# Kernel optimization log

Measured on AMD Instinct MI355X. Metric: run time of the kernel, lower is better.

## Reference

```python
import jax, jax.numpy as jnp
import numpy as np

Q_DIM = 64

def setup_inputs() -> dict:
    key = jax.random.key(0)
    k1, k2, k3, k4 = jax.random.split(key, 4)
    B, T, C, D = 2, 4096, 1024, Q_DIM
    x = jax.random.normal(k1, (B, T, C), dtype=jnp.float32)
    Wq = jax.random.normal(k2, (C, D), dtype=jnp.float32) * (C ** -0.5)
    Wk = jax.random.normal(k3, (C, D), dtype=jnp.float32) * (C ** -0.5)
    Wv = jax.random.normal(k4, (C, D), dtype=jnp.float32) * (C ** -0.5)
    return {"x": x, "Wq": Wq, "Wk": Wk, "Wv": Wv}

def reference(x, Wq, Wk, Wv):
    # x: [B,T,C]; Wq/Wk/Wv: [C,D]
    T = x.shape[1]
    D = Wq.shape[1]
    q = x @ Wq  # [B,T,D]
    k = x @ Wk
    v = x @ Wv
    scale = D ** -0.5
    aff = jnp.einsum('bqd,bkd->bqk', q, k) * scale  # [B,T,T]
    causal = jnp.tril(jnp.ones((T, T), dtype=bool))
    aff = jnp.where(causal, aff, -jnp.inf)
    attn = jax.nn.softmax(aff, axis=-1)
    out = jnp.einsum('bqk,bkd->bqd', attn, v)  # [B,T,D]
    return out
```

## Files before the change

### kernel.cpp

```cpp
#include <hip/hip_runtime.h>

typedef __bf16 bf16_t;
typedef __bf16 bf16x8 __attribute__((ext_vector_type(8)));
typedef __bf16 bf16x4 __attribute__((ext_vector_type(4)));
typedef float  f32x4  __attribute__((ext_vector_type(4)));
typedef _Float16 f16_t;
typedef _Float16 f16x8 __attribute__((ext_vector_type(8)));

#define TSEQ 4096
#define SEGS 8

__device__ __forceinline__ void barrier_lds() {
    __builtin_amdgcn_sched_barrier(0);
    asm volatile("s_waitcnt lgkmcnt(0)" ::: "memory");
    __builtin_amdgcn_s_barrier();
    __builtin_amdgcn_sched_barrier(0);
}

__global__ __launch_bounds__(256) void wsplit_k(
    const float* __restrict__ Wq, const float* __restrict__ Wk,
    const float* __restrict__ Wv, bf16_t* __restrict__ wT)
{
    __shared__ bf16_t th[64][72];
    const int mat = blockIdx.x >> 4;
    const int kb  = (blockIdx.x & 15) * 64;
    const float* W = (mat == 0) ? Wq : ((mat == 1) ? Wk : Wv);
    const float scale = (mat == 0) ? 0.18033688011112042f : 1.0f;
    const int t  = threadIdx.x;
    const int kl = t >> 2;
    const int dc = (t & 3) * 16;
    #pragma unroll
    for (int i = 0; i < 4; ++i) {
        float4 v = *reinterpret_cast<const float4*>(W + (long)(kb + kl) * 64 + dc + 4 * i);
        th[dc + 4*i + 0][kl] = (bf16_t)(v.x * scale);
        th[dc + 4*i + 1][kl] = (bf16_t)(v.y * scale);
        th[dc + 4*i + 2][kl] = (bf16_t)(v.z * scale);
        th[dc + 4*i + 3][kl] = (bf16_t)(v.w * scale);
    }
    __syncthreads();
    const int d  = t >> 2;
    const int kc = (t & 3) * 16;
    bf16x8 a0 = *reinterpret_cast<const bf16x8*>(&th[d][kc]);
    bf16x8 a1 = *reinterpret_cast<const bf16x8*>(&th[d][kc + 8]);
    long o = (long)(mat * 64 + d) * 1024 + kb + kc;
    *reinterpret_cast<bf16x8*>(wT + o)     = a0;
    *reinterpret_cast<bf16x8*>(wT + o + 8) = a1;
}

__global__ __launch_bounds__(256, 2) void proj_mfma(
    const float* __restrict__ X, const bf16_t* __restrict__ wT,
    bf16_t* __restrict__ qh, bf16_t* __restrict__ kh, bf16_t* __restrict__ vt)
{
    __shared__ __align__(16) unsigned char smem[27648];
    bf16_t (*wl)[96][72] = reinterpret_cast<bf16_t(*)[96][72]>(smem);
    float  (*vtl)[36]    = reinterpret_cast<float(*)[36]>(smem);

    const int tid = threadIdx.x, lane = tid & 63;
    const int w   = tid >> 6;
    const int mw  = w >> 1, nw2 = w & 1;
    const int q4 = lane & 15, g = lane >> 4;
    const int bx = blockIdx.x;
    const int rg = bx & 255, nb = bx >> 8;
    const long R0 = (long)rg * 32;

    const float* xrow = X + (R0 + 16 * mw + q4) * 1024 + 8 * g;

    const int wrow = tid >> 1, c32 = (tid & 1) * 32;
    const bf16_t* wsrc = wT + (long)(96 * nb + wrow) * 1024 + c32;
    const bool wact = (tid < 192);

    bf16x8 wr0, wr1, wr2, wr3;
    float4 xE[4], xO[4];
    f32x4 acc[3] = {};

    auto loadW = [&](int t) {
        if (wact) {
            wr0 = *reinterpret_cast<const bf16x8*>(wsrc + t * 64);
            wr1 = *reinterpret_cast<const bf16x8*>(wsrc + t * 64 + 8);
            wr2 = *reinterpret_cast<const bf16x8*>(wsrc + t * 64 + 16);
            wr3 = *reinterpret_cast<const bf16x8*>(wsrc + t * 64 + 24);
        }
    };
    auto writeW = [&](int buf) {
        if (wact) {
            *reinterpret_cast<bf16x8*>(&wl[buf][wrow][c32])      = wr0;
            *reinterpret_cast<bf16x8*>(&wl[buf][wrow][c32 + 8])  = wr1;
            *reinterpret_cast<bf16x8*>(&wl[buf][wrow][c32 + 16]) = wr2;
            *reinterpret_cast<bf16x8*>(&wl[buf][wrow][c32 + 24]) = wr3;
        }
    };
    auto loadX = [&](int t, float4 (&xc)[4]) {
        xc[0] = *reinterpret_cast<const float4*>(xrow + t * 64);
        xc[1] = *reinterpret_cast<const float4*>(xrow + t * 64 + 4);
        xc[2] = *reinterpret_cast<const float4*>(xrow + t * 64 + 32);
        xc[3] = *reinterpret_cast<const float4*>(xrow + t * 64 + 36);
    };

    loadW(0); writeW(0);
    loadW(1);
    loadX(0, xE); loadX(1, xO);
    asm volatile("" ::: "memory");
    barrier_lds();

    auto stepf = [&](int t, float4 (&xc)[4]) {
        if (t + 1 < 16) {
            writeW((t + 1) & 1);
            loadW(t + 2 < 16 ? t + 2 : 15);
        }
        bf16x8 a0 = {(bf16_t)xc[0].x, (bf16_t)xc[0].y, (bf16_t)xc[0].z, (bf16_t)xc[0].w,
                     (bf16_t)xc[1].x, (bf16_t)xc[1].y, (bf16_t)xc[1].z, (bf16_t)xc[1].w};
        bf16x8 a1 = {(bf16_t)xc[2].x, (bf16_t)xc[2].y, (bf16_t)xc[2].z, (bf16_t)xc[2].w,
                     (bf16_t)xc[3].x, (bf16_t)xc[3].y, (bf16_t)xc[3].z, (bf16_t)xc[3].w};
        if (t + 2 < 16) loadX(t + 2, xc);
        asm volatile("" ::: "memory");
        __builtin_amdgcn_s_setprio(1);
        #pragma unroll
        for (int j = 0; j < 3; ++j) {
            const int lr = (3 * nw2 + j) * 16 + q4;
            bf16x8 b0 = *reinterpret_cast<const bf16x8*>(&wl[t & 1][lr][8 * g]);
            bf16x8 b1 = *reinterpret_cast<const bf16x8*>(&wl[t & 1][lr][8 * g + 32]);
            acc[j] = __builtin_amdgcn_mfma_f32_16x16x32_bf16(a0, b0, acc[j], 0, 0, 0);
            acc[j] = __builtin_amdgcn_mfma_f32_16x16x32_bf16(a1, b1, acc[j], 0, 0, 0);
        }
        __builtin_amdgcn_s_setprio(0);
        barrier_lds();
    };
    #pragma unroll
    for (int tt = 0; tt < 16; tt += 2) { stepf(tt, xE); stepf(tt + 1, xO); }

    #pragma unroll
    for (int j = 0; j < 3; ++j) {
        const int nt = 6 * nb + 3 * nw2 + j;
        #pragma unroll
        for (int r = 0; r < 4; ++r) {
            const long row = R0 + 16 * mw + 4 * g + r;
            const float vv = acc[j][r];
            if (nt < 4)      qh[row * 64 + nt * 16 + q4] = (bf16_t)vv;
            else if (nt < 8) kh[row * 64 + (nt - 4) * 16 + q4] = (bf16_t)vv;
            else             vtl[(nt - 8) * 16 + q4][16 * mw + 4 * g + r] = vv;
        }
    }
    if (nb == 1) {
        barrier_lds();
        const int d = tid >> 2, c8 = (tid & 3) * 8;
        bf16x8 o;
        #pragma unroll
        for (int i = 0; i < 8; ++i) o[i] = (bf16_t)vtl[d][c8 + i];
        *reinterpret_cast<bf16x8*>(vt + (long)d * 8192 + R0 + c8) = o;
    }
}

__global__ __launch_bounds__(256, 3) void attn_mfma(
    const bf16_t* __restrict__ qh, const bf16_t* __restrict__ kh,
    const bf16_t* __restrict__ vt,
    f16_t* __restrict__ pO, float* __restrict__ pm, float* __restrict__ pl)
{
    __shared__ __align__(16) unsigned char smem[46080];
    bf16_t (*kl)[64][72]  = reinterpret_cast<bf16_t(*)[64][72]>(smem);
    bf16_t (*vl)[64][72]  = reinterpret_cast<bf16_t(*)[64][72]>(smem + 18432);
    bf16_t (*P)[8][16][8] = reinterpret_cast<bf16_t(*)[8][16][8]>(smem + 36864);
    f16_t  (*ot)[16][72]  = reinterpret_cast<f16_t(*)[16][72]>(smem + 36864);

    const int tid = threadIdx.x, lane = tid & 63, w = tid >> 6;
    const int q4 = lane & 15, g = lane >> 4;
    const int bx = blockIdx.x, b = blockIdx.y;
    const int tile = 63 - (bx >> 3);
    const int seg  = bx & 7;
    const int C = tile + 1;
    if (seg >= C) return;
    const long base = (long)b * TSEQ;
    const int r0 = tile * 64 + 16 * w;

    const bf16_t* qr = qh + (base + r0 + q4) * 64 + 8 * g;
    const bf16x8 qf0 = *reinterpret_cast<const bf16x8*>(qr);
    const bf16x8 qf1 = *reinterpret_cast<const bf16x8*>(qr + 32);

    const int srow = tid >> 2, sc = (tid & 3) * 16;
    const bf16_t* ksrc = kh + (base + srow) * 64 + sc;
    const bf16_t* vsrc = vt + (long)srow * 8192 + base + sc;
    bf16x8 kr0, kr1, vr0, vr1;
    auto loadKV = [&](int kb) {
        kr0 = *reinterpret_cast<const bf16x8*>(ksrc + (long)kb * 64);
        kr1 = *reinterpret_cast<const bf16x8*>(ksrc + (long)kb * 64 + 8);
        vr0 = *reinterpret_cast<const bf16x8*>(vsrc + kb);
        vr1 = *reinterpret_cast<const bf16x8*>(vsrc + kb + 8);
    };
    auto writeKV = [&](int buf) {
        *reinterpret_cast<bf16x8*>(&kl[buf][srow][sc])     = kr0;
        *reinterpret_cast<bf16x8*>(&kl[buf][srow][sc + 8]) = kr1;
        *reinterpret_cast<bf16x8*>(&vl[buf][srow][sc])     = vr0;
        *reinterpret_cast<bf16x8*>(&vl[buf][srow][sc + 8]) = vr1;
    };

    float m = -1e30f, l = 0.f;
    f32x4 oacc[4] = {};

    loadKV(seg << 6);
    writeKV(0);
    { int c1 = seg + SEGS; loadKV((c1 < C ? c1 : seg) << 6); }
    asm volatile("" ::: "memory");
    barrier_lds();

    int i = 0;
    for (int c = seg; c < C; c += SEGS, ++i) {
        const int buf = i & 1;
        if (c + SEGS < C) {
            writeKV(buf ^ 1);
            int cn = c + 2 * SEGS;
            loadKV((cn < C ? cn : c + SEGS) << 6);
            asm volatile("" ::: "memory");
        }
        const int kb = c << 6;

        f32x4 sacc[4];
        __builtin_amdgcn_s_setprio(1);
        #pragma unroll
        for (int kt = 0; kt < 4; ++kt) {
            bf16x8 kf0 = *reinterpret_cast<const bf16x8*>(&kl[buf][kt * 16 + q4][8 * g]);
            bf16x8 kf1 = *reinterpret_cast<const bf16x8*>(&kl[buf][kt * 16 + q4][8 * g + 32]);
            f32x4 a = {};
            a = __builtin_amdgcn_mfma_f32_16x16x32_bf16(kf0, qf0, a, 0, 0, 0);
            a = __builtin_amdgcn_mfma_f32_16x16x32_bf16(kf1, qf1, a, 0, 0, 0);
            sacc[kt] = a;
        }
        __builtin_amdgcn_s_setprio(0);

        float p[16];
        const bool diag = (c == C - 1);
        float mx = -1e30f;
        #pragma unroll
        for (int kt = 0; kt < 4; ++kt)
            #pragma unroll
            for (int r = 0; r < 4; ++r) {
                float sv = sacc[kt][r];
                if (diag && (kb + kt * 16 + 4 * g + r > r0 + q4)) sv = -1e30f;
                p[kt * 4 + r] = sv;
                mx = fmaxf(mx, sv);
            }
        mx = fmaxf(mx, __shfl_xor(mx, 16));
        mx = fmaxf(mx, __shfl_xor(mx, 32));
        const float mnew = fmaxf(m, mx);
        const float alpha = __builtin_exp2f(m - mnew);
        m = mnew;
        float lsum = 0.f;
        #pragma unroll
        for (int ii = 0; ii < 16; ++ii) { p[ii] = __builtin_exp2f(p[ii] - mnew); lsum += p[ii]; }
        lsum += __shfl_xor(lsum, 16);
        lsum += __shfl_xor(lsum, 32);
        l = l * alpha + lsum;
        #pragma unroll
        for (int dt = 0; dt < 4; ++dt) oacc[dt] *= alpha;

        #pragma unroll
        for (int kt = 0; kt < 4; ++kt) {
            const int cb = 2 * kt + (g >> 1);
            const int ki = (g & 1) << 2;
            bf16x4 hv = {(bf16_t)p[4*kt+0], (bf16_t)p[4*kt+1],
                         (bf16_t)p[4*kt+2], (bf16_t)p[4*kt+3]};
            *reinterpret_cast<bf16x4*>(&P[w][cb][q4][ki]) = hv;
        }
        bf16x8 ph0 = *reinterpret_cast<const bf16x8*>(&P[w][g][q4][0]);
        bf16x8 ph1 = *reinterpret_cast<const bf16x8*>(&P[w][4 + g][q4][0]);
        __builtin_amdgcn_s_setprio(1);
        #pragma unroll
        for (int dt = 0; dt < 4; ++dt) {
            bf16x8 va0 = *reinterpret_cast<const bf16x8*>(&vl[buf][dt * 16 + q4][8 * g]);
            bf16x8 va1 = *reinterpret_cast<const bf16x8*>(&vl[buf][dt * 16 + q4][8 * g + 32]);
            oacc[dt] = __builtin_amdgcn_mfma_f32_16x16x32_bf16(va0, ph0, oacc[dt], 0, 0, 0);
            oacc[dt] = __builtin_amdgcn_mfma_f32_16x16x32_bf16(va1, ph1, oacc[dt], 0, 0, 0);
        }
        __builtin_amdgcn_s_setprio(0);
        barrier_lds();
    }

    const float invl = 1.0f / l;
    #pragma unroll
    for (int dt = 0; dt < 4; ++dt)
        #pragma unroll
        for (int r = 0; r < 4; ++r)
            ot[w][q4][dt * 16 + 4 * g + r] = (f16_t)(oacc[dt][r] * invl);

    const long pbase = (((long)b * 64 + tile) * SEGS + seg) * 64;
    {
        const int q  = lane >> 2;
        const int dc = (lane & 3) * 16;
        f16x8 o0 = *reinterpret_cast<const f16x8*>(&ot[w][q][dc]);
        f16x8 o1 = *reinterpret_cast<const f16x8*>(&ot[w][q][dc + 8]);
        f16_t* dst = pO + (pbase + 16 * w + q) * 64 + dc;
        *reinterpret_cast<f16x8*>(dst)     = o0;
        *reinterpret_cast<f16x8*>(dst + 8) = o1;
    }
    if (g == 0) {
        pm[pbase + 16 * w + q4] = m;
        pl[pbase + 16 * w + q4] = l;
    }
}

__global__ __launch_bounds__(256) void merge_k(
    const f16_t* __restrict__ pO, const float* __restrict__ pm,
    const float* __restrict__ pl, float* __restrict__ O)
{
    const int tile = blockIdx.x, b = blockIdx.y;
    const int C = tile + 1;
    const int S = (C < SEGS) ? C : SEGS;
    const int t = threadIdx.x;
    const int q = t >> 2, dc = (t & 3) * 16;
    const long pb = ((long)b * 64 + tile) * SEGS;

    float mstar = -1e30f;
    for (int s = 0; s < S; ++s) mstar = fmaxf(mstar, pm[(pb + s) * 64 + q]);
    float L = 0.f;
    float o[16];
    #pragma unroll
    for (int i = 0; i < 16; ++i) o[i] = 0.f;
    for (int s = 0; s < S; ++s) {
        const float ws = __builtin_exp2f(pm[(pb + s) * 64 + q] - mstar) * pl[(pb + s) * 64 + q];
        L += ws;
        const f16_t* src = pO + ((pb + s) * 64 + q) * 64 + dc;
        f16x8 a0 = *reinterpret_cast<const f16x8*>(src);
        f16x8 a1 = *reinterpret_cast<const f16x8*>(src + 8);
        #pragma unroll
        for (int i = 0; i < 8; ++i) {
            o[i]     += ws * (float)a0[i];
            o[8 + i] += ws * (float)a1[i];
        }
    }
    const float inv = 1.0f / L;
    float* dst = O + ((long)b * TSEQ + tile * 64 + q) * 64 + dc;
    #pragma unroll
    for (int i = 0; i < 4; ++i) {
        f32x4 v = {o[4*i] * inv, o[4*i+1] * inv, o[4*i+2] * inv, o[4*i+3] * inv};
        *reinterpret_cast<f32x4*>(dst + 4 * i) = v;
    }
}

extern "C" void kernel_launch(void* const* d_in, const int* in_sizes, int n_in,
                              void* d_out, int out_size, void* d_ws, size_t ws_size,
                              hipStream_t stream)
{
    const float* X  = (const float*)d_in[0];
    const float* Wq = (const float*)d_in[1];
    const float* Wk = (const float*)d_in[2];
    const float* Wv = (const float*)d_in[3];
    float* O = (float*)d_out;

    char* ws = (char*)d_ws;
    size_t off = 0;
    bf16_t* wT = (bf16_t*)(ws + off); off += 192 * 1024 * sizeof(bf16_t);
    bf16_t* qh = (bf16_t*)(ws + off); off += 8192L * 64 * sizeof(bf16_t);
    bf16_t* kh = (bf16_t*)(ws + off); off += 8192L * 64 * sizeof(bf16_t);
    bf16_t* vt = (bf16_t*)(ws + off); off += 64L * 8192 * sizeof(bf16_t);
    f16_t*  pO = (f16_t*)(ws + off);  off += 2L * 64 * SEGS * 64 * 64 * sizeof(f16_t);
    float*  pm = (float*)(ws + off);  off += 2L * 64 * SEGS * 64 * sizeof(float);
    float*  pl = (float*)(ws + off);  off += 2L * 64 * SEGS * 64 * sizeof(float);

    wsplit_k <<<48, 256, 0, stream>>>(Wq, Wk, Wv, wT);
    proj_mfma<<<512, 256, 0, stream>>>(X, wT, qh, kh, vt);
    attn_mfma<<<dim3(512, 2), 256, 0, stream>>>(qh, kh, vt, pO, pm, pl);
    merge_k  <<<dim3(64, 2), 256, 0, stream>>>(pO, pm, pl, O);
}
```

Baseline: 57.80 us.

## Rework projection tiling, single-buffer attention KV with more segments and lazy rescale

The projection kernel now has each block compute all 192 output columns for 16 rows, so X is read once rather than twice, at the cost of doubling LDS to 55 KB per block. The attention kernel raises the key-split count from 8 to 12, drops KV double-buffering to halve LDS, and lifts the occupancy hint to 5 blocks per CU. It also skips the accumulator rescale when the running max does not change. Single buffering adds a second barrier per iteration and weakens load/compute overlap, and more segments add merge traffic.

```diff
diff --git a/kernel.cpp b/kernel.cpp
--- a/kernel.cpp
+++ b/kernel.cpp
@@ -8,7 +8,7 @@
 typedef _Float16 f16x8 __attribute__((ext_vector_type(8)));
 
 #define TSEQ 4096
-#define SEGS 8
+#define SEGS 12
 
 __device__ __forceinline__ void barrier_lds() {
     __builtin_amdgcn_sched_barrier(0);
@@ -51,43 +51,40 @@
     const float* __restrict__ X, const bf16_t* __restrict__ wT,
     bf16_t* __restrict__ qh, bf16_t* __restrict__ kh, bf16_t* __restrict__ vt)
 {
-    __shared__ __align__(16) unsigned char smem[27648];
-    bf16_t (*wl)[96][72] = reinterpret_cast<bf16_t(*)[96][72]>(smem);
-    float  (*vtl)[36]    = reinterpret_cast<float(*)[36]>(smem);
+    __shared__ __align__(16) unsigned char smem[55296];
+    bf16_t (*wl)[192][72] = reinterpret_cast<bf16_t(*)[192][72]>(smem);
+    float  (*vtl)[20]     = reinterpret_cast<float(*)[20]>(smem);
 
     const int tid = threadIdx.x, lane = tid & 63;
     const int w   = tid >> 6;
-    const int mw  = w >> 1, nw2 = w & 1;
     const int q4 = lane & 15, g = lane >> 4;
-    const int bx = blockIdx.x;
-    const int rg = bx & 255, nb = bx >> 8;
-    const long R0 = (long)rg * 32;
-
-    const float* xrow = X + (R0 + 16 * mw + q4) * 1024 + 8 * g;
-
-    const int wrow = tid >> 1, c32 = (tid & 1) * 32;
-    const bf16_t* wsrc = wT + (long)(96 * nb + wrow) * 1024 + c32;
-    const bool wact = (tid < 192);
-
-    bf16x8 wr0, wr1, wr2, wr3;
+    const long R0 = (long)blockIdx.x * 16;
+
+    const float* xrow = X + (R0 + q4) * 1024 + 8 * g;
+
+    const int trow = tid >> 3, c = (tid & 7) * 8;
+    const bf16_t* wsrc = wT + (long)trow * 1024 + c;
+
+    bf16x8 wr0, wr1, wr2, wr3, wr4, wr5;
     float4 xE[4], xO[4];
     f32x4 acc[3] = {};
 
     auto loadW = [&](int t) {
-        if (wact) {
-            wr0 = *reinterpret_cast<const bf16x8*>(wsrc + t * 64);
-            wr1 = *reinterpret_cast<const bf16x8*>(wsrc + t * 64 + 8);
-            wr2 = *reinterpret_cast<const bf16x8*>(wsrc + t * 64 + 16);
-            wr3 = *reinterpret_cast<const bf16x8*>(wsrc + t * 64 + 24);
-        }
+        const bf16_t* s = wsrc + t * 64;
+        wr0 = *reinterpret_cast<const bf16x8*>(s);
+        wr1 = *reinterpret_cast<const bf16x8*>(s + 32 * 1024);
+        wr2 = *reinterpret_cast<const bf16x8*>(s + 64 * 1024);
+        wr3 = *reinterpret_cast<const bf16x8*>(s + 96 * 1024);
+        wr4 = *reinterpret_cast<const bf16x8*>(s + 128 * 1024);
+        wr5 = *reinterpret_cast<const bf16x8*>(s + 160 * 1024);
     };
     auto writeW = [&](int buf) {
-        if (wact) {
-            *reinterpret_cast<bf16x8*>(&wl[buf][wrow][c32])      = wr0;
-            *reinterpret_cast<bf16x8*>(&wl[buf][wrow][c32 + 8])  = wr1;
-            *reinterpret_cast<bf16x8*>(&wl[buf][wrow][c32 + 16]) = wr2;
-            *reinterpret_cast<bf16x8*>(&wl[buf][wrow][c32 + 24]) = wr3;
-        }
+        *reinterpret_cast<bf16x8*>(&wl[buf][trow      ][c]) = wr0;
+        *reinterpret_cast<bf16x8*>(&wl[buf][trow +  32][c]) = wr1;
+        *reinterpret_cast<bf16x8*>(&wl[buf][trow +  64][c]) = wr2;
+        *reinterpret_cast<bf16x8*>(&wl[buf][trow +  96][c]) = wr3;
+        *reinterpret_cast<bf16x8*>(&wl[buf][trow + 128][c]) = wr4;
+        *reinterpret_cast<bf16x8*>(&wl[buf][trow + 160][c]) = wr5;
     };
     auto loadX = [&](int t, float4 (&xc)[4]) {
         xc[0] = *reinterpret_cast<const float4*>(xrow + t * 64);
@@ -116,7 +113,7 @@
         __builtin_amdgcn_s_setprio(1);
         #pragma unroll
         for (int j = 0; j < 3; ++j) {
-            const int lr = (3 * nw2 + j) * 16 + q4;
+            const int lr = (3 * w + j) * 16 + q4;
             bf16x8 b0 = *reinterpret_cast<const bf16x8*>(&wl[t & 1][lr][8 * g]);
             bf16x8 b1 = *reinterpret_cast<const bf16x8*>(&wl[t & 1][lr][8 * g + 32]);
             acc[j] = __builtin_amdgcn_mfma_f32_16x16x32_bf16(a0, b0, acc[j], 0, 0, 0);
@@ -130,42 +127,42 @@
 
     #pragma unroll
     for (int j = 0; j < 3; ++j) {
-        const int nt = 6 * nb + 3 * nw2 + j;
+        const int nt = 3 * w + j;
         #pragma unroll
         for (int r = 0; r < 4; ++r) {
-            const long row = R0 + 16 * mw + 4 * g + r;
+            const long row = R0 + 4 * g + r;
             const float vv = acc[j][r];
             if (nt < 4)      qh[row * 64 + nt * 16 + q4] = (bf16_t)vv;
             else if (nt < 8) kh[row * 64 + (nt - 4) * 16 + q4] = (bf16_t)vv;
-            else             vtl[(nt - 8) * 16 + q4][16 * mw + 4 * g + r] = vv;
-        }
-    }
-    if (nb == 1) {
-        barrier_lds();
-        const int d = tid >> 2, c8 = (tid & 3) * 8;
-        bf16x8 o;
-        #pragma unroll
-        for (int i = 0; i < 8; ++i) o[i] = (bf16_t)vtl[d][c8 + i];
-        *reinterpret_cast<bf16x8*>(vt + (long)d * 8192 + R0 + c8) = o;
-    }
-}
-
-__global__ __launch_bounds__(256, 3) void attn_mfma(
+            else             vtl[(nt - 8) * 16 + q4][4 * g + r] = vv;
+        }
+    }
+    barrier_lds();
+    {
+        const int d = tid >> 2, rc = (tid & 3) * 4;
+        bf16x4 o;
+        #pragma unroll
+        for (int i = 0; i < 4; ++i) o[i] = (bf16_t)vtl[d][rc + i];
+        *reinterpret_cast<bf16x4*>(vt + (long)d * 8192 + R0 + rc) = o;
+    }
+}
+
+__global__ __launch_bounds__(256, 5) void attn_mfma(
     const bf16_t* __restrict__ qh, const bf16_t* __restrict__ kh,
     const bf16_t* __restrict__ vt,
     f16_t* __restrict__ pO, float* __restrict__ pm, float* __restrict__ pl)
 {
-    __shared__ __align__(16) unsigned char smem[46080];
-    bf16_t (*kl)[64][72]  = reinterpret_cast<bf16_t(*)[64][72]>(smem);
-    bf16_t (*vl)[64][72]  = reinterpret_cast<bf16_t(*)[64][72]>(smem + 18432);
-    bf16_t (*P)[8][16][8] = reinterpret_cast<bf16_t(*)[8][16][8]>(smem + 36864);
-    f16_t  (*ot)[16][72]  = reinterpret_cast<f16_t(*)[16][72]>(smem + 36864);
+    __shared__ __align__(16) unsigned char smem[27648];
+    bf16_t (*kl)[72]      = reinterpret_cast<bf16_t(*)[72]>(smem);
+    bf16_t (*vl)[72]      = reinterpret_cast<bf16_t(*)[72]>(smem + 9216);
+    bf16_t (*P)[8][16][8] = reinterpret_cast<bf16_t(*)[8][16][8]>(smem + 18432);
+    f16_t  (*ot)[16][72]  = reinterpret_cast<f16_t(*)[16][72]>(smem + 18432);
 
     const int tid = threadIdx.x, lane = tid & 63, w = tid >> 6;
     const int q4 = lane & 15, g = lane >> 4;
     const int bx = blockIdx.x, b = blockIdx.y;
-    const int tile = 63 - (bx >> 3);
-    const int seg  = bx & 7;
+    const int tile = 63 - bx / SEGS;
+    const int seg  = bx % SEGS;
     const int C = tile + 1;
     if (seg >= C) return;
     const long base = (long)b * TSEQ;
@@ -185,39 +182,31 @@
         vr0 = *reinterpret_cast<const bf16x8*>(vsrc + kb);
         vr1 = *reinterpret_cast<const bf16x8*>(vsrc + kb + 8);
     };
-    auto writeKV = [&](int buf) {
-        *reinterpret_cast<bf16x8*>(&kl[buf][srow][sc])     = kr0;
-        *reinterpret_cast<bf16x8*>(&kl[buf][srow][sc + 8]) = kr1;
-        *reinterpret_cast<bf16x8*>(&vl[buf][srow][sc])     = vr0;
-        *reinterpret_cast<bf16x8*>(&vl[buf][srow][sc + 8]) = vr1;
+    auto writeKV = [&]() {
+        *reinterpret_cast<bf16x8*>(&kl[srow][sc])     = kr0;
+        *reinterpret_cast<bf16x8*>(&kl[srow][sc + 8]) = kr1;
+        *reinterpret_cast<bf16x8*>(&vl[srow][sc])     = vr0;
+        *reinterpret_cast<bf16x8*>(&vl[srow][sc + 8]) = vr1;
     };
 
     float m = -1e30f, l = 0.f;
     f32x4 oacc[4] = {};
 
     loadKV(seg << 6);
-    writeKV(0);
+    writeKV();
     { int c1 = seg + SEGS; loadKV((c1 < C ? c1 : seg) << 6); }
     asm volatile("" ::: "memory");
     barrier_lds();
 
-    int i = 0;
-    for (int c = seg; c < C; c += SEGS, ++i) {
-        const int buf = i & 1;
-        if (c + SEGS < C) {
-            writeKV(buf ^ 1);
-            int cn = c + 2 * SEGS;
-            loadKV((cn < C ? cn : c + SEGS) << 6);
-            asm volatile("" ::: "memory");
-        }
+    for (int c = seg; c < C; c += SEGS) {
         const int kb = c << 6;
 
         f32x4 sacc[4];
         __builtin_amdgcn_s_setprio(1);
         #pragma unroll
         for (int kt = 0; kt < 4; ++kt) {
-            bf16x8 kf0 = *reinterpret_cast<const bf16x8*>(&kl[buf][kt * 16 + q4][8 * g]);
-            bf16x8 kf1 = *reinterpret_cast<const bf16x8*>(&kl[buf][kt * 16 + q4][8 * g + 32]);
+            bf16x8 kf0 = *reinterpret_cast<const bf16x8*>(&kl[kt * 16 + q4][8 * g]);
+            bf16x8 kf1 = *reinterpret_cast<const bf16x8*>(&kl[kt * 16 + q4][8 * g + 32]);
             f32x4 a = {};
             a = __builtin_amdgcn_mfma_f32_16x16x32_bf16(kf0, qf0, a, 0, 0, 0);
             a = __builtin_amdgcn_mfma_f32_16x16x32_bf16(kf1, qf1, a, 0, 0, 0);
@@ -225,54 +214,83 @@
         }
         __builtin_amdgcn_s_setprio(0);
 
-        float p[16];
-        const bool diag = (c == C - 1);
-        float mx = -1e30f;
+        if (c == C - 1) {
+            const int kk = kb + 4 * g;
+            #pragma unroll
+            for (int kt = 0; kt < 4; ++kt)
+                #pragma unroll
+                for (int r = 0; r < 4; ++r)
+                    if (kk + kt * 16 + r > r0 + q4) sacc[kt][r] = -1e30f;
+        }
+
+        float mx = sacc[0][0];
         #pragma unroll
         for (int kt = 0; kt < 4; ++kt)
             #pragma unroll
-            for (int r = 0; r < 4; ++r) {
-                float sv = sacc[kt][r];
-                if (diag && (kb + kt * 16 + 4 * g + r > r0 + q4)) sv = -1e30f;
-                p[kt * 4 + r] = sv;
-                mx = fmaxf(mx, sv);
-            }
+            for (int r = 0; r < 4; ++r) mx = fmaxf(mx, sacc[kt][r]);
         mx = fmaxf(mx, __shfl_xor(mx, 16));
         mx = fmaxf(mx, __shfl_xor(mx, 32));
-        const float mnew = fmaxf(m, mx);
-        const float alpha = __builtin_exp2f(m - mnew);
-        m = mnew;
+
         float lsum = 0.f;
-        #pragma unroll
-        for (int ii = 0; ii < 16; ++ii) { p[ii] = __builtin_exp2f(p[ii] - mnew); lsum += p[ii]; }
+        if (__all(mx <= m)) {
+            #pragma unroll
+            for (int kt = 0; kt < 4; ++kt)
+                #pragma unroll
+                for (int r = 0; r < 4; ++r) {
+                    sacc[kt][r] = __builtin_exp2f(sacc[kt][r] - m);
+                    lsum += sacc[kt][r];
+                }
+        } else {
+            const float mnew = fmaxf(m, mx);
+            const float alpha = __builtin_exp2f(m - mnew);
+            m = mnew;
+            #pragma unroll
+            for (int kt = 0; kt < 4; ++kt)
+                #pragma unroll
+                for (int r = 0; r < 4; ++r) {
+                    sacc[kt][r] = __builtin_exp2f(sacc[kt][r] - mnew);
+                    lsum += sacc[kt][r];
+                }
+            #pragma unroll
+            for (int dt = 0; dt < 4; ++dt) oacc[dt] *= alpha;
+            l *= alpha;
+        }
         lsum += __shfl_xor(lsum, 16);
         lsum += __shfl_xor(lsum, 32);
-        l = l * alpha + lsum;
-        #pragma unroll
-        for (int dt = 0; dt < 4; ++dt) oacc[dt] *= alpha;
+        l += lsum;
 
         #pragma unroll
         for (int kt = 0; kt < 4; ++kt) {
             const int cb = 2 * kt + (g >> 1);
             const int ki = (g & 1) << 2;
-            bf16x4 hv = {(bf16_t)p[4*kt+0], (bf16_t)p[4*kt+1],
-                         (bf16_t)p[4*kt+2], (bf16_t)p[4*kt+3]};
+            bf16x4 hv = {(bf16_t)sacc[kt][0], (bf16_t)sacc[kt][1],
+                         (bf16_t)sacc[kt][2], (bf16_t)sacc[kt][3]};
             *reinterpret_cast<bf16x4*>(&P[w][cb][q4][ki]) = hv;
         }
         bf16x8 ph0 = *reinterpret_cast<const bf16x8*>(&P[w][g][q4][0]);
         bf16x8 ph1 = *reinterpret_cast<const bf16x8*>(&P[w][4 + g][q4][0]);
+
         __builtin_amdgcn_s_setprio(1);
         #pragma unroll
         for (int dt = 0; dt < 4; ++dt) {
-            bf16x8 va0 = *reinterpret_cast<const bf16x8*>(&vl[buf][dt * 16 + q4][8 * g]);
-            bf16x8 va1 = *reinterpret_cast<const bf16x8*>(&vl[buf][dt * 16 + q4][8 * g + 32]);
+            bf16x8 va0 = *reinterpret_cast<const bf16x8*>(&vl[dt * 16 + q4][8 * g]);
+            bf16x8 va1 = *reinterpret_cast<const bf16x8*>(&vl[dt * 16 + q4][8 * g + 32]);
             oacc[dt] = __builtin_amdgcn_mfma_f32_16x16x32_bf16(va0, ph0, oacc[dt], 0, 0, 0);
             oacc[dt] = __builtin_amdgcn_mfma_f32_16x16x32_bf16(va1, ph1, oacc[dt], 0, 0, 0);
         }
         __builtin_amdgcn_s_setprio(0);
-        barrier_lds();
-    }
-
+
+        if (c + SEGS < C) {
+            barrier_lds();
+            writeKV();
+            int cn = c + 2 * SEGS;
+            loadKV((cn < C ? cn : c + SEGS) << 6);
+            asm volatile("" ::: "memory");
+            barrier_lds();
+        }
+    }
+
+    barrier_lds();
     const float invl = 1.0f / l;
     #pragma unroll
     for (int dt = 0; dt < 4; ++dt)
@@ -356,6 +374,6 @@
 
     wsplit_k <<<48, 256, 0, stream>>>(Wq, Wk, Wv, wT);
     proj_mfma<<<512, 256, 0, stream>>>(X, wT, qh, kh, vt);
-    attn_mfma<<<dim3(512, 2), 256, 0, stream>>>(qh, kh, vt, pO, pm, pl);
+    attn_mfma<<<dim3(64 * SEGS, 2), 256, 0, stream>>>(qh, kh, vt, pO, pm, pl);
     merge_k  <<<dim3(64, 2), 256, 0, stream>>>(pO, pm, pl, O);
 }
```

Measured after the change: 68.90 us. +19.2%, slower.
